# Optimization experiments

Measured on AMD Instinct MI355X. Metric: run time of the kernel, lower is better.

Reference implementation:

```python
import jax, jax.numpy as jnp
import numpy as np

C = 32        # channels
B = 4         # batch
H = W = 256   # spatial
K = 3         # adaptive kernel size
BN_EPS = 1e-5


def conv2d(x, w, b, pad):
    # x: [B,Cin,H,W], w: [Cout,Cin,kh,kw]
    y = jax.lax.conv_general_dilated(
        x, w, window_strides=(1, 1), padding=[(pad, pad), (pad, pad)],
        dimension_numbers=('NCHW', 'OIHW', 'NCHW'))
    return y + b[None, :, None, None]


def bn(x, g, beta, mu, var):
    scale = (g / jnp.sqrt(var + BN_EPS))[None, :, None, None]
    return (x - mu[None, :, None, None]) * scale + beta[None, :, None, None]


def res_block(x, w, b, g, beta, mu, var):
    # w: [2,C,C,3,3]; conv-BN-ReLU-conv-BN, residual add, ReLU
    h = bn(conv2d(x, w[0], b[0], 1), g[0], beta[0], mu[0], var[0])
    h = jax.nn.relu(h)
    h = bn(conv2d(h, w[1], b[1], 1), g[1], beta[1], mu[1], var[1])
    return jax.nn.relu(x + h)


def kernel_pred(frames, core, rate):
    # frames: [B,N,H,W] (color=1 squeezed), core: [B,N,K*K,H,W]
    b, n, h, w = frames.shape
    p = (K // 2) * rate
    fp = jnp.pad(frames, ((0, 0), (0, 0), (p, p), (p, p)))
    # stack K*K shifted copies along new axis 2 (same order as torch loop)
    stack = jnp.stack([fp[:, :, i * rate:i * rate + h, j * rate:j * rate + w]
                       for i in range(K) for j in range(K)], axis=2)
    return jnp.sum(core * stack, axis=2)  # [B,N,H,W]; white_level=1.0


def setup_inputs() -> dict:
    key = jax.random.key(0)
    ks = jax.random.split(key, 16)
    inp = {}
    inp['input'] = jax.random.normal(ks[0], (B, C, H, W), dtype=jnp.float32)
    # 4 residual blocks x 2 convs each
    inp['wconv'] = 0.05 * jax.random.normal(ks[1], (4, 2, C, C, 3, 3), dtype=jnp.float32)
    inp['bconv'] = jnp.zeros((4, 2, C), dtype=jnp.float32)
    inp['bn_gamma'] = jnp.ones((4, 2, C), dtype=jnp.float32) + 0.01 * jax.random.normal(ks[2], (4, 2, C), dtype=jnp.float32)
    inp['bn_beta'] = 0.01 * jax.random.normal(ks[3], (4, 2, C), dtype=jnp.float32)
    inp['bn_mean'] = 0.1 * jax.random.normal(ks[4], (4, 2, C), dtype=jnp.float32)
    inp['bn_var'] = 0.5 + jax.random.uniform(ks[5], (4, 2, C), dtype=jnp.float32)
    inp['tau'] = 0.5 * jnp.ones((1, C, 1, 1), dtype=jnp.float32)
    inp['w_outc'] = 0.05 * jax.random.normal(ks[6], (C * 9, C, 1, 1), dtype=jnp.float32)
    inp['b_outc'] = jnp.zeros((C * 9,), dtype=jnp.float32)
    inp['w_final'] = 0.05 * jax.random.normal(ks[7], (C, C * 4, 3, 3), dtype=jnp.float32)
    inp['b_final'] = jnp.zeros((C,), dtype=jnp.float32)
    return inp


def reference(input, wconv, bconv, bn_gamma, bn_beta, bn_mean, bn_var, tau,
              w_outc, b_outc, w_final, b_final):
    m = input
    for i in range(4):  # fixed small structural loop over residual blocks
        m = res_block(m, wconv[i], bconv[i], bn_gamma[i], bn_beta[i],
                      bn_mean[i], bn_var[i])
    m5 = jax.nn.relu(m - tau)
    core = conv2d(m5, w_outc, b_outc, 0)                    # [B, C*9, H, W]
    core = core.reshape(B, C, K * K, H, W)                  # [B, N, 9, H, W]
    preds = [kernel_pred(input, core, r) for r in (1, 2, 3, 4)]
    pred_cat = jnp.concatenate(preds, axis=1)               # [B, 4C, H, W]
    return conv2d(pred_cat, w_final, b_final, 1)            # [B, C, H, W]
```

## Files before the change

kernel.cpp:

```cpp
#include <hip/hip_runtime.h>

typedef __bf16 bf16;
typedef __attribute__((ext_vector_type(8))) __bf16 bf16x8;
typedef __attribute__((ext_vector_type(4))) float f32x4;

#define HH 256
#define WW 256
#define BB 4
#define NPIX 65536

__device__ inline bf16x8 bzero8() {
    bf16x8 v;
    #pragma unroll
    for (int i = 0; i < 8; ++i) v[i] = (bf16)0.0f;
    return v;
}

__device__ inline int chof(int s) {
    return 4 * (s >> 3) + 16 * ((s >> 2) & 1) + (s & 3);
}

__global__ __launch_bounds__(256) void prep_in(const float* __restrict__ in,
                                               bf16* __restrict__ outP) {
    int p = blockIdx.x * 256 + threadIdx.x;
    int b = p >> 16, rem = p & 65535;
    float ch[32];
    #pragma unroll
    for (int c = 0; c < 32; ++c)
        ch[c] = in[(size_t)(b * 32 + c) * NPIX + rem];
    #pragma unroll
    for (int g = 0; g < 4; ++g) {
        bf16x8 w;
        #pragma unroll
        for (int j = 0; j < 4; ++j) {
            w[j]     = (bf16)ch[4 * g + j];
            w[4 + j] = (bf16)ch[16 + 4 * g + j];
        }
        *reinterpret_cast<bf16x8*>(outP + (size_t)p * 32 + g * 8) = w;
    }
}

__global__ void fold_w(const float* __restrict__ wconv, const float* __restrict__ bconv,
                       const float* __restrict__ g, const float* __restrict__ beta,
                       const float* __restrict__ mu, const float* __restrict__ var,
                       const float* __restrict__ w_outc, const float* __restrict__ b_outc,
                       const float* __restrict__ w_final, const float* __restrict__ tau,
                       bf16* __restrict__ Wres, float* __restrict__ Bres,
                       bf16* __restrict__ Wcore, bf16* __restrict__ Wfin,
                       float* __restrict__ bCore, float* __restrict__ tauP) {
    int idx = blockIdx.x * 256 + threadIdx.x;
    if (idx < 73728) {
        int l = idx / 9216, r = idx % 9216;
        int tap = r >> 10, co = (r >> 5) & 31, ci = chof(r & 31);
        float s = g[l * 32 + co] * rsqrtf(var[l * 32 + co] + 1e-5f);
        Wres[idx] = (bf16)(wconv[l * 9216 + (co * 32 + ci) * 9 + tap] * s);
    } else if (idx < 73984) {
        int i = idx - 73728;
        float s = g[i] * rsqrtf(var[i] + 1e-5f);
        Bres[i] = (bconv[i] - mu[i]) * s + beta[i];
    } else if (idx < 83200) {
        int r = idx - 73984;
        int tap = r >> 10, nn = (r >> 5) & 31, ci = chof(r & 31);
        Wcore[r] = (bf16)w_outc[(nn * 9 + tap) * 32 + ci];
    } else if (idx < 120064) {
        int r = idx - 83200;
        int chunk = r / 9216, r2 = r % 9216;
        int tap = r2 >> 10, co = (r2 >> 5) & 31, n = chof(r2 & 31);
        Wfin[r] = (bf16)w_final[(size_t)(co * 128 + chunk * 32 + n) * 9 + tap];
    } else if (idx < 120352) {
        int r = idx - 120064;
        int tap = r >> 5, n = r & 31;
        bCore[r] = b_outc[n * 9 + tap];
    } else if (idx < 120384) {
        int s = idx - 120352;
        tauP[s] = tau[chof(s)];
    }
}

__global__ __launch_bounds__(512) void resblock_mfma(
    const bf16* __restrict__ in, const bf16* __restrict__ W1,
    const bf16* __restrict__ W2, const float* __restrict__ B1,
    const float* __restrict__ B2, bf16* __restrict__ out) {
    extern __shared__ char smem[];
    bf16* xs = (bf16*)smem;
    bf16* hs = (bf16*)(smem + 65280);
    const int x0 = blockIdx.x * 64, y0 = blockIdx.y * 8, b = blockIdx.z;
    const int tid = threadIdx.x;
    const int lane = tid & 63, wv = tid >> 6;
    const int col = lane & 15, g = lane >> 4;

    const bf16* inb = in + (size_t)b * NPIX * 32;
    for (int i = tid; i < 3264; i += 512) {
        int px = i >> 2, cg = i & 3;
        int yy = px / 68, xx = px % 68;
        int gy = y0 + yy - 2, gx = x0 + xx - 2;
        bf16x8 v = bzero8();
        if ((unsigned)gy < HH && (unsigned)gx < WW)
            v = *reinterpret_cast<const bf16x8*>(inb + ((size_t)gy * WW + gx) * 32 + cg * 8);
        *reinterpret_cast<bf16x8*>(xs + px * 40 + cg * 8) = v;
    }

    bf16x8 Wf[9][2];
    #pragma unroll
    for (int tap = 0; tap < 9; ++tap) {
        Wf[tap][0] = *reinterpret_cast<const bf16x8*>(W1 + tap * 1024 + col * 32 + g * 8);
        Wf[tap][1] = *reinterpret_cast<const bf16x8*>(W1 + tap * 1024 + (16 + col) * 32 + g * 8);
    }
    f32x4 bb0 = *reinterpret_cast<const f32x4*>(B1 + 4 * g);
    f32x4 bb1 = *reinterpret_cast<const f32x4*>(B1 + 16 + 4 * g);
    __syncthreads();

    for (int u = wv; u < 50; u += 8) {
        int r = u / 5, s = u - 5 * r;
        int off = s * 16; if (off > 50) off = 50;
        f32x4 c0 = bb0, c1 = bb1;
        #pragma unroll
        for (int tap = 0; tap < 9; ++tap) {
            const int dy = tap / 3, dx = tap % 3;
            bf16x8 Bf = *reinterpret_cast<const bf16x8*>(
                xs + ((r + dy) * 68 + off + col + dx) * 40 + g * 8);
            c0 = __builtin_amdgcn_mfma_f32_16x16x32_bf16(Wf[tap][0], Bf, c0, 0, 0, 0);
            c1 = __builtin_amdgcn_mfma_f32_16x16x32_bf16(Wf[tap][1], Bf, c1, 0, 0, 0);
        }
        bf16x8 o;
        #pragma unroll
        for (int j = 0; j < 4; ++j) {
            o[j]     = (bf16)fmaxf(c0[j], 0.0f);
            o[4 + j] = (bf16)fmaxf(c1[j], 0.0f);
        }
        const int hy = y0 + r - 1;
        const int hx = x0 + off + col - 1;
        if ((unsigned)hy >= HH || (unsigned)hx >= WW) o = bzero8();
        *reinterpret_cast<bf16x8*>(hs + (r * 66 + off + col) * 40 + g * 8) = o;
    }

    #pragma unroll
    for (int tap = 0; tap < 9; ++tap) {
        Wf[tap][0] = *reinterpret_cast<const bf16x8*>(W2 + tap * 1024 + col * 32 + g * 8);
        Wf[tap][1] = *reinterpret_cast<const bf16x8*>(W2 + tap * 1024 + (16 + col) * 32 + g * 8);
    }
    bb0 = *reinterpret_cast<const f32x4*>(B2 + 4 * g);
    bb1 = *reinterpret_cast<const f32x4*>(B2 + 16 + 4 * g);
    __syncthreads();

    bf16* outb = out + (size_t)b * NPIX * 32;
    #pragma unroll
    for (int sg = 0; sg < 4; ++sg) {
        f32x4 c0 = bb0, c1 = bb1;
        #pragma unroll
        for (int tap = 0; tap < 9; ++tap) {
            const int dy = tap / 3, dx = tap % 3;
            bf16x8 Bf = *reinterpret_cast<const bf16x8*>(
                hs + ((wv + dy) * 66 + sg * 16 + col + dx) * 40 + g * 8);
            c0 = __builtin_amdgcn_mfma_f32_16x16x32_bf16(Wf[tap][0], Bf, c0, 0, 0, 0);
            c1 = __builtin_amdgcn_mfma_f32_16x16x32_bf16(Wf[tap][1], Bf, c1, 0, 0, 0);
        }
        bf16x8 xr = *reinterpret_cast<const bf16x8*>(
            xs + ((wv + 2) * 68 + sg * 16 + col + 2) * 40 + g * 8);
        bf16x8 o;
        #pragma unroll
        for (int j = 0; j < 4; ++j) {
            o[j]     = (bf16)fmaxf(c0[j] + (float)xr[j], 0.0f);
            o[4 + j] = (bf16)fmaxf(c1[j] + (float)xr[4 + j], 0.0f);
        }
        *reinterpret_cast<bf16x8*>(
            outb + ((size_t)(y0 + wv) * WW + x0 + sg * 16 + col) * 32 + g * 8) = o;
    }
}

__global__ __launch_bounds__(256) void final_conv_v2(
    const bf16* __restrict__ pred, const bf16* __restrict__ Wfin,
    const float* __restrict__ bfin, float* __restrict__ out) {
    __shared__ bf16 pt[6 * 66 * 40];
    const int x0 = blockIdx.x * 64, y0 = blockIdx.y * 4, b = blockIdx.z;
    const int tid = threadIdx.x;
    const int lane = tid & 63, wv = tid >> 6;
    const int col = lane & 15, g = lane >> 4;

    f32x4 a0[4], a1[4];
    {
        f32x4 b0 = *reinterpret_cast<const f32x4*>(bfin + 4 * g);
        f32x4 b1 = *reinterpret_cast<const f32x4*>(bfin + 16 + 4 * g);
        #pragma unroll
        for (int i = 0; i < 4; ++i) { a0[i] = b0; a1[i] = b1; }
    }

    const bf16* pb = pred + (size_t)b * NPIX * 128;
    for (int chunk = 0; chunk < 4; ++chunk) {
        if (chunk) __syncthreads();
        for (int i = tid; i < 1584; i += 256) {
            int px = i >> 2, cg = i & 3;
            int yy = px / 66, xx = px % 66;
            int gy = y0 + yy - 1, gx = x0 + xx - 1;
            bf16x8 v = bzero8();
            if ((unsigned)gy < HH && (unsigned)gx < WW)
                v = *reinterpret_cast<const bf16x8*>(
                    pb + ((size_t)gy * WW + gx) * 128 + chunk * 32 + cg * 8);
            *reinterpret_cast<bf16x8*>(pt + px * 40 + cg * 8) = v;
        }
        bf16x8 Wf[9][2];
        #pragma unroll
        for (int tap = 0; tap < 9; ++tap) {
            Wf[tap][0] = *reinterpret_cast<const bf16x8*>(
                Wfin + chunk * 9216 + tap * 1024 + col * 32 + g * 8);
            Wf[tap][1] = *reinterpret_cast<const bf16x8*>(
                Wfin + chunk * 9216 + tap * 1024 + (16 + col) * 32 + g * 8);
        }
        __syncthreads();

        #pragma unroll
        for (int sg = 0; sg < 4; ++sg) {
            #pragma unroll
            for (int tap = 0; tap < 9; ++tap) {
                const int dy = tap / 3, dx = tap % 3;
                bf16x8 Bf = *reinterpret_cast<const bf16x8*>(
                    pt + ((wv + dy) * 66 + sg * 16 + col + dx) * 40 + g * 8);
                a0[sg] = __builtin_amdgcn_mfma_f32_16x16x32_bf16(Wf[tap][0], Bf, a0[sg], 0, 0, 0);
                a1[sg] = __builtin_amdgcn_mfma_f32_16x16x32_bf16(Wf[tap][1], Bf, a1[sg], 0, 0, 0);
            }
        }
    }

    const int y = y0 + wv;
    #pragma unroll
    for (int sg = 0; sg < 4; ++sg) {
        const int x = x0 + sg * 16 + col;
        #pragma unroll
        for (int j = 0; j < 4; ++j) {
            out[(size_t)(b * 32 + 4 * g + j) * NPIX + (size_t)y * WW + x] = a0[sg][j];
            out[(size_t)(b * 32 + 16 + 4 * g + j) * NPIX + (size_t)y * WW + x] = a1[sg][j];
        }
    }
}

__global__ __launch_bounds__(256, 2) void core_pred_v4(
    const bf16* __restrict__ m, const bf16* __restrict__ framesP,
    const float* __restrict__ tauP, const bf16* __restrict__ WcoreG,
    const float* __restrict__ bCore, bf16* __restrict__ pred) {
    __shared__ bf16 fr[576 * 32];
    __shared__ bf16 Wc[9 * 32 * 32];
    const int x0 = blockIdx.x * 16, y0 = blockIdx.y * 16, b = blockIdx.z;
    const int tid = threadIdx.x;
    const int lane = tid & 63, wv = tid >> 6;
    const int col = lane & 15, g = lane >> 4;

    for (int i = tid; i < 1152; i += 256)
        *reinterpret_cast<bf16x8*>(Wc + i * 8) =
            *reinterpret_cast<const bf16x8*>(WcoreG + i * 8);
    const bf16* fb = framesP + (size_t)b * NPIX * 32;
    for (int i = tid; i < 2304; i += 256) {
        int px = i >> 2, cg = i & 3;
        int yy = px / 24, xx = px % 24;
        int gy = y0 + yy - 4, gx = x0 + xx - 4;
        bf16x8 v = bzero8();
        if ((unsigned)gy < HH && (unsigned)gx < WW)
            v = *reinterpret_cast<const bf16x8*>(fb + ((size_t)gy * WW + gx) * 32 + cg * 8);
        *reinterpret_cast<bf16x8*>(fr + px * 32 + cg * 8) = v;
    }
    float t8[8];
    #pragma unroll
    for (int k = 0; k < 8; ++k) t8[k] = tauP[g * 8 + k];
    __syncthreads();

    const bf16* mb = m + (size_t)b * NPIX * 32;
    bf16* pb = pred + (size_t)b * NPIX * 128;

    #pragma unroll 1
    for (int uu = 0; uu < 4; ++uu) {
        const int yl = wv * 4 + uu;
        const int y = y0 + yl;

        bf16x8 Bv = *reinterpret_cast<const bf16x8*>(
            mb + ((size_t)y * WW + x0 + col) * 32 + g * 8);
        #pragma unroll
        for (int k = 0; k < 8; ++k)
            Bv[k] = (bf16)fmaxf((float)Bv[k] - t8[k], 0.0f);

        float acc[4][8];
        #pragma unroll
        for (int r = 0; r < 4; ++r)
            #pragma unroll
            for (int k = 0; k < 8; ++k) acc[r][k] = 0.0f;

        #pragma unroll
        for (int dy = 0; dy < 3; ++dy) {
            float core[3][8];
            #pragma unroll
            for (int dx = 0; dx < 3; ++dx) {
                const int tap = dy * 3 + dx;
                bf16x8 A0 = *reinterpret_cast<const bf16x8*>(
                    Wc + tap * 1024 + col * 32 + g * 8);
                bf16x8 A1 = *reinterpret_cast<const bf16x8*>(
                    Wc + tap * 1024 + (16 + col) * 32 + g * 8);
                f32x4 c0 = *reinterpret_cast<const f32x4*>(bCore + tap * 32 + 4 * g);
                f32x4 c1 = *reinterpret_cast<const f32x4*>(bCore + tap * 32 + 16 + 4 * g);
                c0 = __builtin_amdgcn_mfma_f32_16x16x32_bf16(A0, Bv, c0, 0, 0, 0);
                c1 = __builtin_amdgcn_mfma_f32_16x16x32_bf16(A1, Bv, c1, 0, 0, 0);
                #pragma unroll
                for (int j = 0; j < 4; ++j) {
                    core[dx][j]     = c0[j];
                    core[dx][4 + j] = c1[j];
                }
            }
            #pragma unroll
            for (int r = 1; r <= 4; ++r) {
                const int row = yl + 4 + (dy - 1) * r;
                #pragma unroll
                for (int dx = 0; dx < 3; ++dx) {
                    const int cc = col + 4 + (dx - 1) * r;
                    bf16x8 f8 = *reinterpret_cast<const bf16x8*>(
                        fr + (row * 24 + cc) * 32 + g * 8);
                    #pragma unroll
                    for (int k = 0; k < 8; ++k)
                        acc[r - 1][k] += core[dx][k] * (float)f8[k];
                }
            }
        }

        #pragma unroll
        for (int r = 0; r < 4; ++r) {
            bf16x8 o;
            #pragma unroll
            for (int k = 0; k < 8; ++k) o[k] = (bf16)acc[r][k];
            *reinterpret_cast<bf16x8*>(
                pb + ((size_t)y * WW + x0 + col) * 128 + r * 32 + g * 8) = o;
        }
    }
}

extern "C" void kernel_launch(void* const* d_in, const int* in_sizes, int n_in,
                              void* d_out, int out_size, void* d_ws, size_t ws_size,
                              hipStream_t stream) {
    const float* input    = (const float*)d_in[0];
    const float* wconv    = (const float*)d_in[1];
    const float* bconv    = (const float*)d_in[2];
    const float* bn_gamma = (const float*)d_in[3];
    const float* bn_beta  = (const float*)d_in[4];
    const float* bn_mean  = (const float*)d_in[5];
    const float* bn_var   = (const float*)d_in[6];
    const float* tau      = (const float*)d_in[7];
    const float* w_outc   = (const float*)d_in[8];
    const float* b_outc   = (const float*)d_in[9];
    const float* w_final  = (const float*)d_in[10];
    const float* b_final  = (const float*)d_in[11];
    float* out = (float*)d_out;

    char* ws = (char*)d_ws;
    bf16*  Wres  = (bf16*)(ws);
    float* Bres  = (float*)(ws + 147456);
    bf16*  Wcore = (bf16*)(ws + 148480);
    bf16*  Wfin  = (bf16*)(ws + 166912);
    float* bCore = (float*)(ws + 240640);
    float* tauP  = (float*)(ws + 241792);
    bf16*  in0b  = (bf16*)(ws + 245760);
    bf16*  actA  = (bf16*)(ws + 245760 + 16777216ull);
    bf16*  actB  = (bf16*)(ws + 245760 + 2 * 16777216ull);
    bf16*  pred  = (bf16*)(ws + 245760 + 3 * 16777216ull);

    hipFuncSetAttribute(reinterpret_cast<const void*>(&resblock_mfma),
                        hipFuncAttributeMaxDynamicSharedMemorySize, 118080);

    prep_in<<<1024, 256, 0, stream>>>(input, in0b);
    fold_w<<<471, 256, 0, stream>>>(wconv, bconv, bn_gamma, bn_beta, bn_mean, bn_var,
                                    w_outc, b_outc, w_final, tau,
                                    Wres, Bres, Wcore, Wfin, bCore, tauP);

    dim3 grid(4, 32, 4), blk(512);
    resblock_mfma<<<grid, blk, 118080, stream>>>(in0b, Wres + 0 * 9216, Wres + 1 * 9216,
                                                 Bres + 0,  Bres + 32,  actA);
    resblock_mfma<<<grid, blk, 118080, stream>>>(actA, Wres + 2 * 9216, Wres + 3 * 9216,
                                                 Bres + 64, Bres + 96,  actB);
    resblock_mfma<<<grid, blk, 118080, stream>>>(actB, Wres + 4 * 9216, Wres + 5 * 9216,
                                                 Bres + 128, Bres + 160, actA);
    resblock_mfma<<<grid, blk, 118080, stream>>>(actA, Wres + 6 * 9216, Wres + 7 * 9216,
                                                 Bres + 192, Bres + 224, actB);

    dim3 gridp(16, 16, 4);
    core_pred_v4<<<gridp, dim3(256), 0, stream>>>(actB, in0b, tauP, Wcore, bCore, pred);

    dim3 gridf(4, 64, 4);
    final_conv_v2<<<gridf, dim3(256), 0, stream>>>(pred, Wfin, b_final, out);
}
```

Measured before the change: 191.5 us.

## Read conv input directly from global memory instead of staging halo tiles in LDS

The residual-block and final-conv kernels no longer stage input halo tiles in shared memory. Each MFMA B-fragment is now loaded straight from global memory with clamped coordinates and zero-masking at the image borders. The residual block is also retiled to 4 output rows with 256 threads and a smaller static LDS buffer for the intermediate activation, which should allow more blocks per CU. This removes the staging loops and barriers but makes each input pixel be fetched up to 9 times through the cache, and the first conv's halo recomputation overhead grows relative to the smaller tile.

```diff
diff --git a/kernel.cpp b/kernel.cpp
--- a/kernel.cpp
+++ b/kernel.cpp
@@ -77,28 +77,16 @@
     }
 }
 
-__global__ __launch_bounds__(512) void resblock_mfma(
+__global__ __launch_bounds__(256) void resblock_v3(
     const bf16* __restrict__ in, const bf16* __restrict__ W1,
     const bf16* __restrict__ W2, const float* __restrict__ B1,
     const float* __restrict__ B2, bf16* __restrict__ out) {
-    extern __shared__ char smem[];
-    bf16* xs = (bf16*)smem;
-    bf16* hs = (bf16*)(smem + 65280);
-    const int x0 = blockIdx.x * 64, y0 = blockIdx.y * 8, b = blockIdx.z;
+    __shared__ bf16 hs[6 * 66 * 40];
+    const int x0 = blockIdx.x * 64, y0 = blockIdx.y * 4, b = blockIdx.z;
     const int tid = threadIdx.x;
     const int lane = tid & 63, wv = tid >> 6;
     const int col = lane & 15, g = lane >> 4;
-
     const bf16* inb = in + (size_t)b * NPIX * 32;
-    for (int i = tid; i < 3264; i += 512) {
-        int px = i >> 2, cg = i & 3;
-        int yy = px / 68, xx = px % 68;
-        int gy = y0 + yy - 2, gx = x0 + xx - 2;
-        bf16x8 v = bzero8();
-        if ((unsigned)gy < HH && (unsigned)gx < WW)
-            v = *reinterpret_cast<const bf16x8*>(inb + ((size_t)gy * WW + gx) * 32 + cg * 8);
-        *reinterpret_cast<bf16x8*>(xs + px * 40 + cg * 8) = v;
-    }
 
     bf16x8 Wf[9][2];
     #pragma unroll
@@ -108,17 +96,21 @@
     }
     f32x4 bb0 = *reinterpret_cast<const f32x4*>(B1 + 4 * g);
     f32x4 bb1 = *reinterpret_cast<const f32x4*>(B1 + 16 + 4 * g);
-    __syncthreads();
-
-    for (int u = wv; u < 50; u += 8) {
+
+    for (int u = wv; u < 30; u += 4) {
         int r = u / 5, s = u - 5 * r;
         int off = s * 16; if (off > 50) off = 50;
+        const int hy = y0 + r - 1;
+        const int hx = x0 + off + col - 1;
         f32x4 c0 = bb0, c1 = bb1;
         #pragma unroll
         for (int tap = 0; tap < 9; ++tap) {
             const int dy = tap / 3, dx = tap % 3;
+            const int gy = hy + dy - 1, gx = hx + dx - 1;
+            const int cy = min(max(gy, 0), HH - 1), cx = min(max(gx, 0), WW - 1);
             bf16x8 Bf = *reinterpret_cast<const bf16x8*>(
-                xs + ((r + dy) * 68 + off + col + dx) * 40 + g * 8);
+                inb + ((size_t)cy * WW + cx) * 32 + g * 8);
+            if ((unsigned)gy >= HH || (unsigned)gx >= WW) Bf = bzero8();
             c0 = __builtin_amdgcn_mfma_f32_16x16x32_bf16(Wf[tap][0], Bf, c0, 0, 0, 0);
             c1 = __builtin_amdgcn_mfma_f32_16x16x32_bf16(Wf[tap][1], Bf, c1, 0, 0, 0);
         }
@@ -128,8 +120,6 @@
             o[j]     = (bf16)fmaxf(c0[j], 0.0f);
             o[4 + j] = (bf16)fmaxf(c1[j], 0.0f);
         }
-        const int hy = y0 + r - 1;
-        const int hx = x0 + off + col - 1;
         if ((unsigned)hy >= HH || (unsigned)hx >= WW) o = bzero8();
         *reinterpret_cast<bf16x8*>(hs + (r * 66 + off + col) * 40 + g * 8) = o;
     }
@@ -144,6 +134,7 @@
     __syncthreads();
 
     bf16* outb = out + (size_t)b * NPIX * 32;
+    const int y = y0 + wv;
     #pragma unroll
     for (int sg = 0; sg < 4; ++sg) {
         f32x4 c0 = bb0, c1 = bb1;
@@ -156,7 +147,7 @@
             c1 = __builtin_amdgcn_mfma_f32_16x16x32_bf16(Wf[tap][1], Bf, c1, 0, 0, 0);
         }
         bf16x8 xr = *reinterpret_cast<const bf16x8*>(
-            xs + ((wv + 2) * 68 + sg * 16 + col + 2) * 40 + g * 8);
+            inb + ((size_t)y * WW + x0 + sg * 16 + col) * 32 + g * 8);
         bf16x8 o;
         #pragma unroll
         for (int j = 0; j < 4; ++j) {
@@ -164,14 +155,13 @@
             o[4 + j] = (bf16)fmaxf(c1[j] + (float)xr[4 + j], 0.0f);
         }
         *reinterpret_cast<bf16x8*>(
-            outb + ((size_t)(y0 + wv) * WW + x0 + sg * 16 + col) * 32 + g * 8) = o;
-    }
-}
-
-__global__ __launch_bounds__(256) void final_conv_v2(
+            outb + ((size_t)y * WW + x0 + sg * 16 + col) * 32 + g * 8) = o;
+    }
+}
+
+__global__ __launch_bounds__(256) void final_conv_v4(
     const bf16* __restrict__ pred, const bf16* __restrict__ Wfin,
     const float* __restrict__ bfin, float* __restrict__ out) {
-    __shared__ bf16 pt[6 * 66 * 40];
     const int x0 = blockIdx.x * 64, y0 = blockIdx.y * 4, b = blockIdx.z;
     const int tid = threadIdx.x;
     const int lane = tid & 63, wv = tid >> 6;
@@ -186,18 +176,8 @@
     }
 
     const bf16* pb = pred + (size_t)b * NPIX * 128;
+    const int y = y0 + wv;
     for (int chunk = 0; chunk < 4; ++chunk) {
-        if (chunk) __syncthreads();
-        for (int i = tid; i < 1584; i += 256) {
-            int px = i >> 2, cg = i & 3;
-            int yy = px / 66, xx = px % 66;
-            int gy = y0 + yy - 1, gx = x0 + xx - 1;
-            bf16x8 v = bzero8();
-            if ((unsigned)gy < HH && (unsigned)gx < WW)
-                v = *reinterpret_cast<const bf16x8*>(
-                    pb + ((size_t)gy * WW + gx) * 128 + chunk * 32 + cg * 8);
-            *reinterpret_cast<bf16x8*>(pt + px * 40 + cg * 8) = v;
-        }
         bf16x8 Wf[9][2];
         #pragma unroll
         for (int tap = 0; tap < 9; ++tap) {
@@ -206,22 +186,22 @@
             Wf[tap][1] = *reinterpret_cast<const bf16x8*>(
                 Wfin + chunk * 9216 + tap * 1024 + (16 + col) * 32 + g * 8);
         }
-        __syncthreads();
-
         #pragma unroll
         for (int sg = 0; sg < 4; ++sg) {
             #pragma unroll
             for (int tap = 0; tap < 9; ++tap) {
                 const int dy = tap / 3, dx = tap % 3;
+                const int gy = y + dy - 1, gx = x0 + sg * 16 + col + dx - 1;
+                const int cy = min(max(gy, 0), HH - 1), cx = min(max(gx, 0), WW - 1);
                 bf16x8 Bf = *reinterpret_cast<const bf16x8*>(
-                    pt + ((wv + dy) * 66 + sg * 16 + col + dx) * 40 + g * 8);
+                    pb + ((size_t)cy * WW + cx) * 128 + chunk * 32 + g * 8);
+                if ((unsigned)gy >= HH || (unsigned)gx >= WW) Bf = bzero8();
                 a0[sg] = __builtin_amdgcn_mfma_f32_16x16x32_bf16(Wf[tap][0], Bf, a0[sg], 0, 0, 0);
                 a1[sg] = __builtin_amdgcn_mfma_f32_16x16x32_bf16(Wf[tap][1], Bf, a1[sg], 0, 0, 0);
             }
         }
     }
 
-    const int y = y0 + wv;
     #pragma unroll
     for (int sg = 0; sg < 4; ++sg) {
         const int x = x0 + sg * 16 + col;
@@ -357,27 +337,24 @@
     bf16*  actB  = (bf16*)(ws + 245760 + 2 * 16777216ull);
     bf16*  pred  = (bf16*)(ws + 245760 + 3 * 16777216ull);
 
-    hipFuncSetAttribute(reinterpret_cast<const void*>(&resblock_mfma),
-                        hipFuncAttributeMaxDynamicSharedMemorySize, 118080);
-
     prep_in<<<1024, 256, 0, stream>>>(input, in0b);
     fold_w<<<471, 256, 0, stream>>>(wconv, bconv, bn_gamma, bn_beta, bn_mean, bn_var,
                                     w_outc, b_outc, w_final, tau,
                                     Wres, Bres, Wcore, Wfin, bCore, tauP);
 
-    dim3 grid(4, 32, 4), blk(512);
-    resblock_mfma<<<grid, blk, 118080, stream>>>(in0b, Wres + 0 * 9216, Wres + 1 * 9216,
-                                                 Bres + 0,  Bres + 32,  actA);
-    resblock_mfma<<<grid, blk, 118080, stream>>>(actA, Wres + 2 * 9216, Wres + 3 * 9216,
-                                                 Bres + 64, Bres + 96,  actB);
-    resblock_mfma<<<grid, blk, 118080, stream>>>(actB, Wres + 4 * 9216, Wres + 5 * 9216,
-                                                 Bres + 128, Bres + 160, actA);
-    resblock_mfma<<<grid, blk, 118080, stream>>>(actA, Wres + 6 * 9216, Wres + 7 * 9216,
-                                                 Bres + 192, Bres + 224, actB);
+    dim3 grid(4, 64, 4), blk(256);
+    resblock_v3<<<grid, blk, 0, stream>>>(in0b, Wres + 0 * 9216, Wres + 1 * 9216,
+                                          Bres + 0,  Bres + 32,  actA);
+    resblock_v3<<<grid, blk, 0, stream>>>(actA, Wres + 2 * 9216, Wres + 3 * 9216,
+                                          Bres + 64, Bres + 96,  actB);
+    resblock_v3<<<grid, blk, 0, stream>>>(actB, Wres + 4 * 9216, Wres + 5 * 9216,
+                                          Bres + 128, Bres + 160, actA);
+    resblock_v3<<<grid, blk, 0, stream>>>(actA, Wres + 6 * 9216, Wres + 7 * 9216,
+                                          Bres + 192, Bres + 224, actB);
 
     dim3 gridp(16, 16, 4);
     core_pred_v4<<<gridp, dim3(256), 0, stream>>>(actB, in0b, tauP, Wcore, bCore, pred);
 
     dim3 gridf(4, 64, 4);
-    final_conv_v2<<<gridf, dim3(256), 0, stream>>>(pred, Wfin, b_final, out);
-}
+    final_conv_v4<<<gridf, dim3(256), 0, stream>>>(pred, Wfin, b_final, out);
+}
```

Result: slower. 339.3 us (+77.2%).
